# Kernel optimization log

Hardware: AMD Instinct MI355X
Metric: run time of the kernel (lower is better)

The kernel has to match this reference:

```python
import jax, jax.numpy as jnp
import numpy as np

B = 512        # batch size
NCLASS = 128   # number of classes == embedding dim (per module docstring)
K = 8          # topk hard mining
MARGIN = 1.0
P = 1.0 / NCLASS  # default p = 1/nclass


def _pairwise_distances(x):
    # Euclidean distance matrix, with the zero-distance sqrt-safety trick
    dot = x @ x.T                      # (B, B)
    sq = jnp.diag(dot)                 # (B,)
    d = sq[None, :] - 2.0 * dot + sq[:, None]
    d = jnp.maximum(d, 0.0)
    zmask = (d == 0.0).astype(x.dtype)
    return (1.0 - zmask) * jnp.sqrt(d + zmask * 1e-16)


def _topk_rows_mask(valid):
    # torch .topk(k, dim=0, largest=True) + scatter_(0, idx, True):
    # per column, mark the k rows with the largest values.
    _, idx = jax.lax.top_k(valid.T, K)                 # (B, K): row indices per column
    mT = jnp.zeros((B, B), dtype=bool).at[jnp.arange(B)[:, None], idx].set(True)
    return mT.T                                        # back to (row, col) layout


def _forward(x, target):
    d = _pairwise_distances(x)                         # (B, B)
    sim = target[None, :] == target[:, None]           # (B, B) same-class mask

    # hard positives: largest same-class distances per column
    hard_pos = _topk_rows_mask(jnp.where(sim, d, -jnp.inf)) & sim
    # hard negatives: smallest different-class distances per column
    hard_neg = _topk_rows_mask(-jnp.where(sim, jnp.inf, d)) & (~sim)

    # minor-class anchors: class count < int(p * batch)
    boundary = int(P * B)
    cnt = jnp.zeros((NCLASS,), dtype=jnp.int32).at[target].add(1)
    anchors = cnt[target] < boundary                   # (B,)

    eye = jnp.eye(B, dtype=bool)
    mask_ap = (~eye) & anchors[:, None] & hard_pos     # (B, B)
    mask_an = anchors[:, None] & hard_neg              # (B, B)

    # O(B^3) triplet tensor
    t = d[:, :, None] - d[:, None, :] + MARGIN         # (B, B, B)
    m = mask_ap[:, :, None] & mask_an[:, None, :]
    t = jnp.maximum(m.astype(x.dtype) * t, 0.0)
    num_pos = jnp.sum(t > 1e-7).astype(x.dtype)
    return jnp.sum(t) / (num_pos + 1e-7)


def setup_inputs() -> dict:
    key = jax.random.key(0)
    k1, k2 = jax.random.split(key)
    x = jax.random.normal(k1, (B, NCLASS), dtype=jnp.float32)
    target = jax.random.randint(k2, (B,), 0, NCLASS)
    return {"x": x, "target": target}


def reference(x, target):
    return _forward(x, target)
```

## Files before the change

### kernel.cpp

```cpp
#include <hip/hip_runtime.h>
#include <math.h>

#define BB 512
#define DD 128
#define KK 8
#define BOUNDARY 4


__global__ __launch_bounds__(512, 4) void fused_kernel(
    const float* __restrict__ x, const int* __restrict__ tgt,
    float* __restrict__ partS, int* __restrict__ partC)
{
    __shared__ float4 xi4[DD / 4];
    __shared__ float s_vn[BB];
    __shared__ float s_sq[BB];
    __shared__ int   s_tgt[BB];
    __shared__ int   s_cnt[128];
    __shared__ int   s_sel[KK];
    __shared__ int   s_pr[16], s_pj[16];
    __shared__ int   s_np;

    int k = blockIdx.x;
    int t = threadIdx.x;
    if (t < DD / 4) xi4[t] = ((const float4*)(x + k * DD))[t];
    if (t < 128) s_cnt[t] = 0;
    if (t == 0) s_np = 0;
    s_tgt[t] = tgt[t];
    __syncthreads();
    int tk = s_tgt[k];

    float z0 = 0.f, z1 = 0.f, z2 = 0.f, z3 = 0.f;
    for (int c = 0; c < DD / 4; ++c) {
        float4 a = xi4[c];
        z0 += a.x * a.x; z1 += a.y * a.y; z2 += a.z * a.z; z3 += a.w * a.w;
    }
    float sqk = (z0 + z1) + (z2 + z3);

    {
        int g = t >> 3, sub = t & 7;
        for (int pass = 0; pass < 4; ++pass) {
            int r0 = pass * 128 + g;
            int r1 = r0 + 64;
            const float4* xr0 = (const float4*)(x + r0 * DD);
            const float4* xr1 = (const float4*)(x + r1 * DD);
            float4 a0 = xi4[sub], a1 = xi4[sub + 8], a2 = xi4[sub + 16], a3 = xi4[sub + 24];
            float4 p0 = xr0[sub], p1 = xr0[sub + 8], p2 = xr0[sub + 16], p3 = xr0[sub + 24];
            float4 q0 = xr1[sub], q1 = xr1[sub + 8], q2 = xr1[sub + 16], q3 = xr1[sub + 24];

            float dA0 = a0.x*p0.x + a0.y*p0.y + a0.z*p0.z + a0.w*p0.w;
            float sA0 = p0.x*p0.x + p0.y*p0.y + p0.z*p0.z + p0.w*p0.w;
            float dA1 = a1.x*p1.x + a1.y*p1.y + a1.z*p1.z + a1.w*p1.w;
            float sA1 = p1.x*p1.x + p1.y*p1.y + p1.z*p1.z + p1.w*p1.w;
            float dA2 = a2.x*p2.x + a2.y*p2.y + a2.z*p2.z + a2.w*p2.w;
            float sA2 = p2.x*p2.x + p2.y*p2.y + p2.z*p2.z + p2.w*p2.w;
            float dA3 = a3.x*p3.x + a3.y*p3.y + a3.z*p3.z + a3.w*p3.w;
            float sA3 = p3.x*p3.x + p3.y*p3.y + p3.z*p3.z + p3.w*p3.w;

            float dB0 = a0.x*q0.x + a0.y*q0.y + a0.z*q0.z + a0.w*q0.w;
            float sB0 = q0.x*q0.x + q0.y*q0.y + q0.z*q0.z + q0.w*q0.w;
            float dB1 = a1.x*q1.x + a1.y*q1.y + a1.z*q1.z + a1.w*q1.w;
            float sB1 = q1.x*q1.x + q1.y*q1.y + q1.z*q1.z + q1.w*q1.w;
            float dB2 = a2.x*q2.x + a2.y*q2.y + a2.z*q2.z + a2.w*q2.w;
            float sB2 = q2.x*q2.x + q2.y*q2.y + q2.z*q2.z + q2.w*q2.w;
            float dB3 = a3.x*q3.x + a3.y*q3.y + a3.z*q3.z + a3.w*q3.w;
            float sB3 = q3.x*q3.x + q3.y*q3.y + q3.z*q3.z + q3.w*q3.w;

            float dotA = (dA0 + dA1) + (dA2 + dA3);
            float sqA  = (sA0 + sA1) + (sA2 + sA3);
            float dotB = (dB0 + dB1) + (dB2 + dB3);
            float sqB  = (sB0 + sB1) + (sB2 + sB3);
            for (int off = 4; off > 0; off >>= 1) {
                dotA += __shfl_down(dotA, off, 8);
                sqA  += __shfl_down(sqA,  off, 8);
                dotB += __shfl_down(dotB, off, 8);
                sqB  += __shfl_down(sqB,  off, 8);
            }
            if (sub == 0) {
                float dsqA = fmaxf((sqk + sqA) - 2.f * dotA, 0.f);
                float dvA = (dsqA == 0.f) ? 0.f : sqrtf(dsqA);
                s_sq[r0] = sqA;
                s_vn[r0] = (s_tgt[r0] == tk) ? -INFINITY : -dvA;
                float dsqB = fmaxf((sqk + sqB) - 2.f * dotB, 0.f);
                float dvB = (dsqB == 0.f) ? 0.f : sqrtf(dsqB);
                s_sq[r1] = sqB;
                s_vn[r1] = (s_tgt[r1] == tk) ? -INFINITY : -dvB;
            }
        }
    }
    __syncthreads();

    int wave = t >> 6, lane = t & 63;
    if (wave == 0) {
        float v[8];
#pragma unroll
        for (int q = 0; q < 8; ++q) v[q] = s_vn[q * 64 + lane];
        for (int pass = 0; pass < KK; ++pass) {
            float bv = -INFINITY; int bq = -1;
#pragma unroll
            for (int q = 0; q < 8; ++q)
                if (v[q] > bv) { bv = v[q]; bq = q; }
            int bi = (bq >= 0) ? (bq * 64 + lane) : (1 << 30);
            for (int off = 32; off > 0; off >>= 1) {
                float ov = __shfl_down(bv, off);
                int   oi = __shfl_down(bi, off);
                if (ov > bv || (ov == bv && oi < bi)) { bv = ov; bi = oi; }
            }
            bv = __shfl(bv, 0); bi = __shfl(bi, 0);
            if (lane == 0) s_sel[pass] = (bv == -INFINITY) ? -1 : bi;
            const int  popq = bi >> 6;
            const bool mine = ((bi & 63) == lane);
#pragma unroll
            for (int q = 0; q < 8; ++q)
                if (mine && q == popq) v[q] = -INFINITY;
        }
    } else if (wave == 1) {
#pragma unroll
        for (int q = 0; q < 8; ++q) atomicAdd(&s_cnt[s_tgt[q * 64 + lane]], 1);
    }
    __syncthreads();

    {
        int r = s_sel[wave];
        if (r >= 0) {
            int tr = s_tgt[r];
            if (s_cnt[tr] < BOUNDARY) {
                for (int j = lane; j < BB; j += 64)
                    if (j != r && s_tgt[j] == tr) {
                        int idx = atomicAdd(&s_np, 1);
                        s_pr[idx] = r; s_pj[idx] = j;
                    }
            }
        }
    }
    __syncthreads();

    float s = 0.f; int c = 0;
    if (t < s_np) {
        int r = s_pr[t], j = s_pj[t];
        const float4* xr = (const float4*)(x + r * DD);
        const float4* xj = (const float4*)(x + j * DD);
        float d0 = 0.f, d1 = 0.f, d2 = 0.f, d3 = 0.f;
        for (int cc = 0; cc < DD / 4; ++cc) {
            float4 a = xr[cc], b = xj[cc];
            d0 += a.x * b.x; d1 += a.y * b.y; d2 += a.z * b.z; d3 += a.w * b.w;
        }
        float dot = (d0 + d1) + (d2 + d3);
        float dsq = fmaxf((s_sq[r] + s_sq[j]) - 2.f * dot, 0.f);
        float dpos = (dsq == 0.f) ? 0.f : sqrtf(dsq);
        float tv = dpos + s_vn[r] + 1.0f;
        if (tv > 0.f) { s = tv; c = (tv > 1e-7f) ? 1 : 0; }
    }
    if (wave == 0) {
        for (int off = 32; off > 0; off >>= 1) {
            s += __shfl_down(s, off);
            c += __shfl_down(c, off);
        }
        if (lane == 0) { partS[k] = s; partC[k] = c; }
    }
}

__global__ __launch_bounds__(64) void fin_kernel(
    const float* __restrict__ partS, const int* __restrict__ partC,
    float* __restrict__ out)
{
    int lane = threadIdx.x;
    const float4* pS = (const float4*)partS;
    const int4*   pC = (const int4*)partC;
    float4 a = pS[lane], b = pS[lane + 64];
    int4   u = pC[lane], v = pC[lane + 64];
    float S = ((a.x + a.y) + (a.z + a.w)) + ((b.x + b.y) + (b.z + b.w));
    int   C = ((u.x + u.y) + (u.z + u.w)) + ((v.x + v.y) + (v.z + v.w));
    for (int off = 32; off > 0; off >>= 1) {
        S += __shfl_down(S, off);
        C += __shfl_down(C, off);
    }
    if (lane == 0) out[0] = S / ((float)C + 1e-7f);
}

extern "C" void kernel_launch(void* const* d_in, const int* in_sizes, int n_in,
                              void* d_out, int out_size, void* d_ws, size_t ws_size,
                              hipStream_t stream) {
    const float* x   = (const float*)d_in[0];
    const int*   tgt = (const int*)d_in[1];
    float* out = (float*)d_out;

    char* ws = (char*)d_ws;
    float* partS = (float*)(ws + 0);
    int*   partC = (int*)(ws + 2048);

    fused_kernel<<<BB, 512, 0, stream>>>(x, tgt, partS, partC);
    fin_kernel<<<1, 64, 0, stream>>>(partS, partC, out);
}
```

Before: 70.73 us.

## Process two anchor columns per block to reuse row loads

Each block now handles two columns (anchors), computing distances for both against every row from a single pass over x. The two top-k selections run in parallel on separate waves, and two waves each compute the triplet sums for one column. This halves the grid and the redundant global reads of x and the per-row norms, at the cost of more registers per thread and a lower launch-bounds occupancy hint.

```diff
diff --git a/kernel.cpp b/kernel.cpp
--- a/kernel.cpp
+++ b/kernel.cpp
@@ -7,34 +7,46 @@
 #define BOUNDARY 4
 
 
-__global__ __launch_bounds__(512, 4) void fused_kernel(
+__global__ __launch_bounds__(512, 2) void fused2_kernel(
     const float* __restrict__ x, const int* __restrict__ tgt,
     float* __restrict__ partS, int* __restrict__ partC)
 {
-    __shared__ float4 xi4[DD / 4];
-    __shared__ float s_vn[BB];
+    __shared__ float4 xiA[DD / 4], xiB[DD / 4];
+    __shared__ float s_vnA[BB], s_vnB[BB];
     __shared__ float s_sq[BB];
     __shared__ int   s_tgt[BB];
     __shared__ int   s_cnt[128];
-    __shared__ int   s_sel[KK];
-    __shared__ int   s_pr[16], s_pj[16];
-    __shared__ int   s_np;
-
-    int k = blockIdx.x;
-    int t = threadIdx.x;
-    if (t < DD / 4) xi4[t] = ((const float4*)(x + k * DD))[t];
+    __shared__ int   s_selA[KK], s_selB[KK];
+    __shared__ int   s_prA[16], s_pjA[16], s_prB[16], s_pjB[16];
+    __shared__ int   s_npA, s_npB;
+
+    const int cA = blockIdx.x * 2, cB = cA + 1;
+    const int t = threadIdx.x;
+    if (t < DD / 4)             xiA[t]      = ((const float4*)(x + cA * DD))[t];
+    else if (t < DD / 2)        xiB[t - 32] = ((const float4*)(x + cB * DD))[t - 32];
     if (t < 128) s_cnt[t] = 0;
-    if (t == 0) s_np = 0;
+    if (t == 0) { s_npA = 0; s_npB = 0; }
     s_tgt[t] = tgt[t];
     __syncthreads();
-    int tk = s_tgt[k];
-
-    float z0 = 0.f, z1 = 0.f, z2 = 0.f, z3 = 0.f;
-    for (int c = 0; c < DD / 4; ++c) {
-        float4 a = xi4[c];
-        z0 += a.x * a.x; z1 += a.y * a.y; z2 += a.z * a.z; z3 += a.w * a.w;
-    }
-    float sqk = (z0 + z1) + (z2 + z3);
+    const int tkA = s_tgt[cA], tkB = s_tgt[cB];
+
+    float sqkA, sqkB;
+    {
+        float z0 = 0.f, z1 = 0.f, z2 = 0.f, z3 = 0.f;
+        for (int c = 0; c < DD / 4; ++c) {
+            float4 a = xiA[c];
+            z0 += a.x * a.x; z1 += a.y * a.y; z2 += a.z * a.z; z3 += a.w * a.w;
+        }
+        sqkA = (z0 + z1) + (z2 + z3);
+    }
+    {
+        float z0 = 0.f, z1 = 0.f, z2 = 0.f, z3 = 0.f;
+        for (int c = 0; c < DD / 4; ++c) {
+            float4 a = xiB[c];
+            z0 += a.x * a.x; z1 += a.y * a.y; z2 += a.z * a.z; z3 += a.w * a.w;
+        }
+        sqkB = (z0 + z1) + (z2 + z3);
+    }
 
     {
         int g = t >> 3, sub = t & 7;
@@ -43,57 +55,71 @@
             int r1 = r0 + 64;
             const float4* xr0 = (const float4*)(x + r0 * DD);
             const float4* xr1 = (const float4*)(x + r1 * DD);
-            float4 a0 = xi4[sub], a1 = xi4[sub + 8], a2 = xi4[sub + 16], a3 = xi4[sub + 24];
+            float4 aA0 = xiA[sub], aA1 = xiA[sub + 8], aA2 = xiA[sub + 16], aA3 = xiA[sub + 24];
+            float4 aB0 = xiB[sub], aB1 = xiB[sub + 8], aB2 = xiB[sub + 16], aB3 = xiB[sub + 24];
             float4 p0 = xr0[sub], p1 = xr0[sub + 8], p2 = xr0[sub + 16], p3 = xr0[sub + 24];
             float4 q0 = xr1[sub], q1 = xr1[sub + 8], q2 = xr1[sub + 16], q3 = xr1[sub + 24];
 
-            float dA0 = a0.x*p0.x + a0.y*p0.y + a0.z*p0.z + a0.w*p0.w;
+            float dA0 = aA0.x*p0.x + aA0.y*p0.y + aA0.z*p0.z + aA0.w*p0.w;
+            float dA1 = aA1.x*p1.x + aA1.y*p1.y + aA1.z*p1.z + aA1.w*p1.w;
+            float dA2 = aA2.x*p2.x + aA2.y*p2.y + aA2.z*p2.z + aA2.w*p2.w;
+            float dA3 = aA3.x*p3.x + aA3.y*p3.y + aA3.z*p3.z + aA3.w*p3.w;
+            float bA0 = aB0.x*p0.x + aB0.y*p0.y + aB0.z*p0.z + aB0.w*p0.w;
+            float bA1 = aB1.x*p1.x + aB1.y*p1.y + aB1.z*p1.z + aB1.w*p1.w;
+            float bA2 = aB2.x*p2.x + aB2.y*p2.y + aB2.z*p2.z + aB2.w*p2.w;
+            float bA3 = aB3.x*p3.x + aB3.y*p3.y + aB3.z*p3.z + aB3.w*p3.w;
             float sA0 = p0.x*p0.x + p0.y*p0.y + p0.z*p0.z + p0.w*p0.w;
-            float dA1 = a1.x*p1.x + a1.y*p1.y + a1.z*p1.z + a1.w*p1.w;
             float sA1 = p1.x*p1.x + p1.y*p1.y + p1.z*p1.z + p1.w*p1.w;
-            float dA2 = a2.x*p2.x + a2.y*p2.y + a2.z*p2.z + a2.w*p2.w;
             float sA2 = p2.x*p2.x + p2.y*p2.y + p2.z*p2.z + p2.w*p2.w;
-            float dA3 = a3.x*p3.x + a3.y*p3.y + a3.z*p3.z + a3.w*p3.w;
             float sA3 = p3.x*p3.x + p3.y*p3.y + p3.z*p3.z + p3.w*p3.w;
-
-            float dB0 = a0.x*q0.x + a0.y*q0.y + a0.z*q0.z + a0.w*q0.w;
+            float dB0 = aA0.x*q0.x + aA0.y*q0.y + aA0.z*q0.z + aA0.w*q0.w;
+            float dB1 = aA1.x*q1.x + aA1.y*q1.y + aA1.z*q1.z + aA1.w*q1.w;
+            float dB2 = aA2.x*q2.x + aA2.y*q2.y + aA2.z*q2.z + aA2.w*q2.w;
+            float dB3 = aA3.x*q3.x + aA3.y*q3.y + aA3.z*q3.z + aA3.w*q3.w;
+            float bB0 = aB0.x*q0.x + aB0.y*q0.y + aB0.z*q0.z + aB0.w*q0.w;
+            float bB1 = aB1.x*q1.x + aB1.y*q1.y + aB1.z*q1.z + aB1.w*q1.w;
+            float bB2 = aB2.x*q2.x + aB2.y*q2.y + aB2.z*q2.z + aB2.w*q2.w;
+            float bB3 = aB3.x*q3.x + aB3.y*q3.y + aB3.z*q3.z + aB3.w*q3.w;
             float sB0 = q0.x*q0.x + q0.y*q0.y + q0.z*q0.z + q0.w*q0.w;
-            float dB1 = a1.x*q1.x + a1.y*q1.y + a1.z*q1.z + a1.w*q1.w;
             float sB1 = q1.x*q1.x + q1.y*q1.y + q1.z*q1.z + q1.w*q1.w;
-            float dB2 = a2.x*q2.x + a2.y*q2.y + a2.z*q2.z + a2.w*q2.w;
             float sB2 = q2.x*q2.x + q2.y*q2.y + q2.z*q2.z + q2.w*q2.w;
-            float dB3 = a3.x*q3.x + a3.y*q3.y + a3.z*q3.z + a3.w*q3.w;
             float sB3 = q3.x*q3.x + q3.y*q3.y + q3.z*q3.z + q3.w*q3.w;
 
-            float dotA = (dA0 + dA1) + (dA2 + dA3);
-            float sqA  = (sA0 + sA1) + (sA2 + sA3);
-            float dotB = (dB0 + dB1) + (dB2 + dB3);
-            float sqB  = (sB0 + sB1) + (sB2 + sB3);
+            float dotA0 = (dA0 + dA1) + (dA2 + dA3);
+            float dotB0 = (bA0 + bA1) + (bA2 + bA3);
+            float sq0   = (sA0 + sA1) + (sA2 + sA3);
+            float dotA1 = (dB0 + dB1) + (dB2 + dB3);
+            float dotB1 = (bB0 + bB1) + (bB2 + bB3);
+            float sq1   = (sB0 + sB1) + (sB2 + sB3);
             for (int off = 4; off > 0; off >>= 1) {
-                dotA += __shfl_down(dotA, off, 8);
-                sqA  += __shfl_down(sqA,  off, 8);
-                dotB += __shfl_down(dotB, off, 8);
-                sqB  += __shfl_down(sqB,  off, 8);
+                dotA0 += __shfl_down(dotA0, off, 8);
+                dotB0 += __shfl_down(dotB0, off, 8);
+                sq0   += __shfl_down(sq0,   off, 8);
+                dotA1 += __shfl_down(dotA1, off, 8);
+                dotB1 += __shfl_down(dotB1, off, 8);
+                sq1   += __shfl_down(sq1,   off, 8);
             }
             if (sub == 0) {
-                float dsqA = fmaxf((sqk + sqA) - 2.f * dotA, 0.f);
-                float dvA = (dsqA == 0.f) ? 0.f : sqrtf(dsqA);
-                s_sq[r0] = sqA;
-                s_vn[r0] = (s_tgt[r0] == tk) ? -INFINITY : -dvA;
-                float dsqB = fmaxf((sqk + sqB) - 2.f * dotB, 0.f);
-                float dvB = (dsqB == 0.f) ? 0.f : sqrtf(dsqB);
-                s_sq[r1] = sqB;
-                s_vn[r1] = (s_tgt[r1] == tk) ? -INFINITY : -dvB;
-            }
-        }
-    }
-    __syncthreads();
-
-    int wave = t >> 6, lane = t & 63;
+                s_sq[r0] = sq0;
+                s_sq[r1] = sq1;
+                float qA0 = fmaxf((sqkA + sq0) - 2.f * dotA0, 0.f);
+                s_vnA[r0] = (s_tgt[r0] == tkA) ? -INFINITY : -((qA0 == 0.f) ? 0.f : sqrtf(qA0));
+                float qB0 = fmaxf((sqkB + sq0) - 2.f * dotB0, 0.f);
+                s_vnB[r0] = (s_tgt[r0] == tkB) ? -INFINITY : -((qB0 == 0.f) ? 0.f : sqrtf(qB0));
+                float qA1 = fmaxf((sqkA + sq1) - 2.f * dotA1, 0.f);
+                s_vnA[r1] = (s_tgt[r1] == tkA) ? -INFINITY : -((qA1 == 0.f) ? 0.f : sqrtf(qA1));
+                float qB1 = fmaxf((sqkB + sq1) - 2.f * dotB1, 0.f);
+                s_vnB[r1] = (s_tgt[r1] == tkB) ? -INFINITY : -((qB1 == 0.f) ? 0.f : sqrtf(qB1));
+            }
+        }
+    }
+    __syncthreads();
+
+    const int wave = t >> 6, lane = t & 63;
     if (wave == 0) {
         float v[8];
 #pragma unroll
-        for (int q = 0; q < 8; ++q) v[q] = s_vn[q * 64 + lane];
+        for (int q = 0; q < 8; ++q) v[q] = s_vnA[q * 64 + lane];
         for (int pass = 0; pass < KK; ++pass) {
             float bv = -INFINITY; int bq = -1;
 #pragma unroll
@@ -106,7 +132,7 @@
                 if (ov > bv || (ov == bv && oi < bi)) { bv = ov; bi = oi; }
             }
             bv = __shfl(bv, 0); bi = __shfl(bi, 0);
-            if (lane == 0) s_sel[pass] = (bv == -INFINITY) ? -1 : bi;
+            if (lane == 0) s_selA[pass] = (bv == -INFINITY) ? -1 : bi;
             const int  popq = bi >> 6;
             const bool mine = ((bi & 63) == lane);
 #pragma unroll
@@ -114,48 +140,89 @@
                 if (mine && q == popq) v[q] = -INFINITY;
         }
     } else if (wave == 1) {
+        float v[8];
+#pragma unroll
+        for (int q = 0; q < 8; ++q) v[q] = s_vnB[q * 64 + lane];
+        for (int pass = 0; pass < KK; ++pass) {
+            float bv = -INFINITY; int bq = -1;
+#pragma unroll
+            for (int q = 0; q < 8; ++q)
+                if (v[q] > bv) { bv = v[q]; bq = q; }
+            int bi = (bq >= 0) ? (bq * 64 + lane) : (1 << 30);
+            for (int off = 32; off > 0; off >>= 1) {
+                float ov = __shfl_down(bv, off);
+                int   oi = __shfl_down(bi, off);
+                if (ov > bv || (ov == bv && oi < bi)) { bv = ov; bi = oi; }
+            }
+            bv = __shfl(bv, 0); bi = __shfl(bi, 0);
+            if (lane == 0) s_selB[pass] = (bv == -INFINITY) ? -1 : bi;
+            const int  popq = bi >> 6;
+            const bool mine = ((bi & 63) == lane);
+#pragma unroll
+            for (int q = 0; q < 8; ++q)
+                if (mine && q == popq) v[q] = -INFINITY;
+        }
+    } else if (wave == 2) {
 #pragma unroll
         for (int q = 0; q < 8; ++q) atomicAdd(&s_cnt[s_tgt[q * 64 + lane]], 1);
     }
     __syncthreads();
 
     {
-        int r = s_sel[wave];
+        int r = s_selA[wave];
         if (r >= 0) {
             int tr = s_tgt[r];
             if (s_cnt[tr] < BOUNDARY) {
                 for (int j = lane; j < BB; j += 64)
                     if (j != r && s_tgt[j] == tr) {
-                        int idx = atomicAdd(&s_np, 1);
-                        s_pr[idx] = r; s_pj[idx] = j;
+                        int idx = atomicAdd(&s_npA, 1);
+                        s_prA[idx] = r; s_pjA[idx] = j;
                     }
             }
         }
-    }
-    __syncthreads();
-
-    float s = 0.f; int c = 0;
-    if (t < s_np) {
-        int r = s_pr[t], j = s_pj[t];
-        const float4* xr = (const float4*)(x + r * DD);
-        const float4* xj = (const float4*)(x + j * DD);
-        float d0 = 0.f, d1 = 0.f, d2 = 0.f, d3 = 0.f;
-        for (int cc = 0; cc < DD / 4; ++cc) {
-            float4 a = xr[cc], b = xj[cc];
-            d0 += a.x * b.x; d1 += a.y * b.y; d2 += a.z * b.z; d3 += a.w * b.w;
-        }
-        float dot = (d0 + d1) + (d2 + d3);
-        float dsq = fmaxf((s_sq[r] + s_sq[j]) - 2.f * dot, 0.f);
-        float dpos = (dsq == 0.f) ? 0.f : sqrtf(dsq);
-        float tv = dpos + s_vn[r] + 1.0f;
-        if (tv > 0.f) { s = tv; c = (tv > 1e-7f) ? 1 : 0; }
-    }
-    if (wave == 0) {
+        r = s_selB[wave];
+        if (r >= 0) {
+            int tr = s_tgt[r];
+            if (s_cnt[tr] < BOUNDARY) {
+                for (int j = lane; j < BB; j += 64)
+                    if (j != r && s_tgt[j] == tr) {
+                        int idx = atomicAdd(&s_npB, 1);
+                        s_prB[idx] = r; s_pjB[idx] = j;
+                    }
+            }
+        }
+    }
+    __syncthreads();
+
+    if (wave < 2) {
+        const int   np  = (wave == 0) ? s_npA : s_npB;
+        const int*  pr  = (wave == 0) ? s_prA : s_prB;
+        const int*  pj  = (wave == 0) ? s_pjA : s_pjB;
+        const float* vn = (wave == 0) ? s_vnA : s_vnB;
+        float s = 0.f; int c = 0;
+        if (lane < np) {
+            int r = pr[lane], j = pj[lane];
+            const float4* xr = (const float4*)(x + r * DD);
+            const float4* xj = (const float4*)(x + j * DD);
+            float d0 = 0.f, d1 = 0.f, d2 = 0.f, d3 = 0.f;
+            for (int cc = 0; cc < DD / 4; ++cc) {
+                float4 a = xr[cc], b = xj[cc];
+                d0 += a.x * b.x; d1 += a.y * b.y; d2 += a.z * b.z; d3 += a.w * b.w;
+            }
+            float dot = (d0 + d1) + (d2 + d3);
+            float dsq = fmaxf((s_sq[r] + s_sq[j]) - 2.f * dot, 0.f);
+            float dpos = (dsq == 0.f) ? 0.f : sqrtf(dsq);
+            float tv = dpos + vn[r] + 1.0f;
+            if (tv > 0.f) { s = tv; c = (tv > 1e-7f) ? 1 : 0; }
+        }
         for (int off = 32; off > 0; off >>= 1) {
             s += __shfl_down(s, off);
             c += __shfl_down(c, off);
         }
-        if (lane == 0) { partS[k] = s; partC[k] = c; }
+        if (lane == 0) {
+            int col = (wave == 0) ? cA : cB;
+            partS[col] = s; partC[col] = c;
+        }
     }
 }
 
@@ -188,6 +255,6 @@
     float* partS = (float*)(ws + 0);
     int*   partC = (int*)(ws + 2048);
 
-    fused_kernel<<<BB, 512, 0, stream>>>(x, tgt, partS, partC);
+    fused2_kernel<<<BB / 2, 512, 0, stream>>>(x, tgt, partS, partC);
     fin_kernel<<<1, 64, 0, stream>>>(partS, partC, out);
 }
```

After: 73.25 us. +3.6%, slower.
